# Kernel tuning notes

Measured on AMD Instinct MI355X. Metric: run time of the kernel, lower is better.

Reference implementation:

```python
import jax, jax.numpy as jnp
import numpy as np

S, B, T = 128, 1024, 96
E, H, HH, ATT = 64, 200, 100, 200
ACT, FLD = 32, 8
V_SRC, N_PROD, V_PRIM, N_FLD = 20000, 101, 10000, 64
DEC_IN = ACT + ATT + FLD + H  # 440


def setup_inputs() -> dict:
    key = jax.random.key(0)
    ks = jax.random.split(key, 24)
    rn = lambda k, shp: jax.random.normal(k, shp, dtype=jnp.float32) * 0.05
    sentences = jax.random.randint(ks[0], (S, B), 0, V_SRC)
    is_prod = jax.random.randint(ks[1], (T, B), 0, 2).astype(jnp.int32)
    prod_ids = jax.random.randint(ks[2], (T, B), 0, N_PROD)
    prim_ids = jax.random.randint(ks[3], (T, B), 0, V_PRIM)
    field_ids = jax.random.randint(ks[4], (T, B), 0, N_FLD)
    pt = jax.random.randint(ks[5], (T, B), 0, T)
    parent_t = jnp.minimum(pt, jnp.maximum(jnp.arange(T)[:, None] - 1, 0))  # parent < t
    return {
        'sentences': sentences, 'is_prod': is_prod, 'prod_ids': prod_ids,
        'prim_ids': prim_ids, 'field_ids': field_ids, 'parent_t': parent_t,
        'src_emb': rn(ks[6], (V_SRC, E)),
        'actprod_emb': rn(ks[7], (N_PROD, ACT)),
        'prim_emb': rn(ks[8], (V_PRIM, ACT)),
        'field_emb': rn(ks[9], (N_FLD, FLD)),
        'Wih_f': rn(ks[10], (4 * HH, E)), 'Whh_f': rn(ks[11], (4 * HH, HH)), 'b_f': rn(ks[12], (4 * HH,)),
        'Wih_b': rn(ks[13], (4 * HH, E)), 'Whh_b': rn(ks[14], (4 * HH, HH)), 'b_b': rn(ks[15], (4 * HH,)),
        'Wih_d': rn(ks[16], (4 * H, DEC_IN)), 'Whh_d': rn(ks[17], (4 * H, H)), 'b_d': rn(ks[18], (4 * H,)),
        'W_attn': rn(ks[19], (H, H)),
        'W_av': rn(ks[20], (ATT, 2 * H)),
    }


def _lstm_cell(z, c):
    i, f, g, o = jnp.split(z, 4, axis=-1)  # torch gate order i,f,g,o
    c = jax.nn.sigmoid(f) * c + jax.nn.sigmoid(i) * jnp.tanh(g)
    h = jax.nn.sigmoid(o) * jnp.tanh(c)
    return h, c


def _lstm_dir(x_emb, Wih, Whh, b, reverse):
    # x_emb: [S,B,E]; precompute input projections once
    xw = jnp.einsum('sbe,he->sbh', x_emb, Wih) + b
    nb = x_emb.shape[1]
    hh = Whh.shape[1]
    init = (jnp.zeros((nb, hh), x_emb.dtype), jnp.zeros((nb, hh), x_emb.dtype))
    def step(carry, xw_t):
        h, c = carry
        h, c = _lstm_cell(xw_t + h @ Whh.T, c)
        return (h, c), h
    (hT, cT), hs = jax.lax.scan(step, init, xw, reverse=reverse)
    return hs, hT, cT


def _forward(sentences, is_prod, prod_ids, prim_ids, field_ids, parent_t,
             src_emb, actprod_emb, prim_emb, field_emb,
             Wih_f, Whh_f, b_f, Wih_b, Whh_b, b_b,
             Wih_d, Whh_d, b_d, W_attn, W_av):
    nb = sentences.shape[1]
    nt = is_prod.shape[0]
    emb = src_emb[sentences]                       # [S,B,E]
    hs_f, hTf, cTf = _lstm_dir(emb, Wih_f, Whh_f, b_f, False)
    hs_b, hTb, cTb = _lstm_dir(emb, Wih_b, Whh_b, b_b, True)
    enc = jnp.concatenate([hs_f, hs_b], -1).transpose(1, 0, 2)   # [B,S,H]
    enc_att = enc @ W_attn.T                                     # [B,S,H]
    # replicate torch h0.view(-1, H) on [2,B,HH]
    h = jnp.stack([hTf, hTb]).reshape(-1, H)
    c = jnp.stack([cTf, cTb]).reshape(-1, H)
    Hbuf = jnp.zeros((nt, nb, H), enc.dtype)
    s_att0 = jnp.zeros((nb, ATT), enc.dtype)
    barange = jnp.arange(nb)

    def dec_step(carry, xs):
        h, c, s_att, Hbuf = carry
        t, ip, pid, prid, fid, ptid = xs
        a_tm1 = jnp.where(ip[:, None] == 1, actprod_emb[pid], prim_emb[prid])  # [B,32]
        nft = field_emb[fid]                                                   # [B,8]
        parent = Hbuf[ptid, barange]                                           # [B,H] irregular gather
        inp = jnp.concatenate([a_tm1, s_att, nft, parent], axis=-1)           # [B,440]
        inp = jnp.where(t > 0, inp, jnp.zeros_like(inp))
        h, c = _lstm_cell(inp @ Wih_d.T + h @ Whh_d.T + b_d, c)
        aw = jax.nn.softmax(jnp.einsum('bsh,bh->bs', enc_att, h), axis=-1)
        ctx = jnp.einsum('bs,bsh->bh', aw, enc)
        s_att = jnp.tanh(jnp.concatenate([ctx, h], axis=1) @ W_av.T)
        Hbuf = Hbuf.at[t].set(h)
        return (h, c, s_att, Hbuf), s_att

    xs = (jnp.arange(nt), is_prod, prod_ids, prim_ids, field_ids, parent_t)
    _, att_vecs = jax.lax.scan(dec_step, (h, c, s_att0, Hbuf), xs)
    return att_vecs  # [T,B,ATT]


def reference(sentences, is_prod, prod_ids, prim_ids, field_ids, parent_t,
              src_emb, actprod_emb, prim_emb, field_emb,
              Wih_f, Whh_f, b_f, Wih_b, Whh_b, b_b,
              Wih_d, Whh_d, b_d, W_attn, W_av):
    return _forward(sentences, is_prod, prod_ids, prim_ids, field_ids, parent_t,
                    src_emb, actprod_emb, prim_emb, field_emb,
                    Wih_f, Whh_f, b_f, Wih_b, Whh_b, b_b,
                    Wih_d, Whh_d, b_d, W_attn, W_av)
```

## Files before the change

### kernel.cpp

```cpp
#include <hip/hip_runtime.h>

#define S_LEN 128
#define B_N   1024
#define T_LEN 96
#define E_DIM 64
#define HH    100
#define H_DIM 200
#define ACT_D 32
#define FLD_D 8
#define ATT_D 200
#define DEC_IN 440
#define KTOT  640
#define G4H   800
#define G4HH  400
#define KH_PAD 224
#define KC_PAD 416
#define NCOL_PAD 208
#define EK_ROWS 208
#define XA_LD 648
#define HG_LD 232
#define GA_LD 232
#define CAT_LD 424

typedef unsigned int  u32;
typedef unsigned short u16;
typedef _Float16 f16;
typedef _Float16 f16x8 __attribute__((ext_vector_type(8)));
typedef _Float16 f16x4 __attribute__((ext_vector_type(4)));
typedef float    f32x4 __attribute__((ext_vector_type(4)));

#define MFMA16(a,b,c) __builtin_amdgcn_mfma_f32_16x16x32_f16((a),(b),(c),0,0,0)

static __device__ __forceinline__ float lo_bf(u32 u){ union{u32 i; float f;}v; v.i = u<<16; return v.f; }
static __device__ __forceinline__ float hi_bf(u32 u){ union{u32 i; float f;}v; v.i = u & 0xffff0000u; return v.f; }
static __device__ __forceinline__ float sigf(float x){
  x = fminf(30.f, fmaxf(-30.f, x));
  return 1.f/(1.f + __expf(-x));
}
static __device__ __forceinline__ float tanhf_(float x){
  x = fminf(15.f, fmaxf(-15.f, x));
  float e = __expf(-2.f*x);
  return (1.f - e)/(1.f + e);
}

static __device__ __forceinline__ u16 f2bf(float f){
  union{float f; u32 i;} v; v.f = f;
  u32 r = v.i + 0x7fffu + ((v.i >> 16) & 1u);
  return (u16)(r >> 16);
}
__global__ void k_prep(u16* __restrict__ dst, const float* __restrict__ src,
                       int K, int C, int sk, int sc)
{
  int idx = blockIdx.x*256 + threadIdx.x;
  if (idx >= K*C) return;
  int k = idx / C, c = idx - k*C;
  dst[(size_t)(k>>2)*(4*C) + 4*c + (k&3)] = f2bf(src[(size_t)k*sk + (size_t)c*sc]);
}

__global__ void k_pack16(f16* __restrict__ dst, const float* __restrict__ src,
                         int Kld, int koff, int C, int K, int sk, int sc)
{
  int idx = blockIdx.x*256 + threadIdx.x;
  if (idx >= C*K) return;
  int c = idx / K, k = idx - c*K;
  dst[(size_t)c*Kld + koff + k] = (f16)src[(size_t)k*sk + (size_t)c*sc];
}

__global__ void k_zf16(f16* __restrict__ dst, int n)
{
  int idx = blockIdx.x*256 + threadIdx.x;
  if (idx < n) dst[idx] = (f16)0.f;
}

__global__ __launch_bounds__(256) void k_transpose(
    const f16* __restrict__ enc_sk, f16* __restrict__ enc_ks)
{
  __shared__ f16 ld[H_DIM][136];
  const int b = blockIdx.x, tid = threadIdx.x;
  const f16* src = enc_sk + (size_t)b*S_LEN*H_DIM;
  for (int idx = tid; idx < S_LEN*(H_DIM/4); idx += 256) {
    int s = idx / (H_DIM/4), jc = idx - s*(H_DIM/4);
    f16x4 v = *(const f16x4*)(src + (size_t)s*H_DIM + 4*jc);
    #pragma unroll
    for (int i = 0; i < 4; ++i) ld[4*jc + i][s] = v[i];
  }
  __syncthreads();
  f16* dst = enc_ks + (size_t)b*EK_ROWS*S_LEN;
  for (int idx = tid; idx < H_DIM*(S_LEN/8); idx += 256) {
    int k = idx / (S_LEN/8), so = idx - k*(S_LEN/8);
    f16x8 v;
    #pragma unroll
    for (int i = 0; i < 8; ++i) v[i] = ld[k][8*so + i];
    *(f16x8*)(dst + (size_t)k*S_LEN + 8*so) = v;
  }
}

__global__ __launch_bounds__(512) void k_encoder(
    const int* __restrict__ sentences, const float* __restrict__ src_emb,
    const float* __restrict__ b_f, const float* __restrict__ b_b,
    const uint2* __restrict__ wihF, const uint2* __restrict__ whhF,
    const uint2* __restrict__ wihB, const uint2* __restrict__ whhB,
    f16* __restrict__ enc_sk,
    float* __restrict__ hTf, float* __restrict__ cTf,
    float* __restrict__ hTb, float* __restrict__ cTb)
{
  const int tid = threadIdx.x;
  const int dir = blockIdx.x >> 7;
  const int bg  = blockIdx.x & 127;
  const int b0  = bg * 8;

  __shared__ alignas(16) float xs[8][E_DIM];
  __shared__ alignas(16) float hs[8][HH];
  __shared__ alignas(16) float zs[8][G4HH];

  const uint2* wih = dir ? wihB : wihF;
  const uint2* whh = dir ? whhB : whhF;
  const float* bias = dir ? b_b : b_f;

  for (int idx = tid; idx < 8*HH; idx += 512) ((float*)hs)[idx] = 0.f;
  float c0r = 0.f, c1r = 0.f;

  const int col = tid;
  const bool act = (col < G4HH);
  const float bias0 = act ? bias[col] : 0.f;

  __syncthreads();

  for (int step = 0; step < S_LEN; ++step) {
    const int s = dir ? (S_LEN-1-step) : step;
    {
      int r = tid >> 6, e = tid & 63;
      int tok = sentences[s*B_N + (b0 + r)];
      xs[r][e] = src_emb[(size_t)tok*E_DIM + e];
    }
    __syncthreads();

    if (act) {
      float acc[8];
      #pragma unroll
      for (int r = 0; r < 8; ++r) acc[r] = bias0;
      #pragma unroll 2
      for (int k4 = 0; k4 < E_DIM/4; ++k4) {
        uint2 u = wih[k4*G4HH + col];
        float w0 = lo_bf(u.x), w1 = hi_bf(u.x), w2 = lo_bf(u.y), w3 = hi_bf(u.y);
        #pragma unroll
        for (int r = 0; r < 8; ++r) {
          float4 xv = *(const float4*)&xs[r][4*k4];
          acc[r] += xv.x*w0 + xv.y*w1 + xv.z*w2 + xv.w*w3;
        }
      }
      #pragma unroll 2
      for (int k4 = 0; k4 < HH/4; ++k4) {
        uint2 u = whh[k4*G4HH + col];
        float w0 = lo_bf(u.x), w1 = hi_bf(u.x), w2 = lo_bf(u.y), w3 = hi_bf(u.y);
        #pragma unroll
        for (int r = 0; r < 8; ++r) {
          float4 hv = *(const float4*)&hs[r][4*k4];
          acc[r] += hv.x*w0 + hv.y*w1 + hv.z*w2 + hv.w*w3;
        }
      }
      #pragma unroll
      for (int r = 0; r < 8; ++r) zs[r][col] = acc[r];
    }
    __syncthreads();

    {
      int r = tid / HH, j = tid - r*HH;
      float c = sigf(zs[r][HH+j])*c0r + sigf(zs[r][j])*tanhf_(zs[r][2*HH+j]);
      float h = sigf(zs[r][3*HH+j])*tanhf_(c);
      c0r = c;
      hs[r][j] = h;
      enc_sk[((size_t)(b0+r)*S_LEN + s)*H_DIM + dir*HH + j] = (f16)h;
      if (tid < 8*HH - 512) {
        int idx2 = tid + 512;
        int r2 = idx2 / HH, j2 = idx2 - r2*HH;
        float c2 = sigf(zs[r2][HH+j2])*c1r + sigf(zs[r2][j2])*tanhf_(zs[r2][2*HH+j2]);
        float h2 = sigf(zs[r2][3*HH+j2])*tanhf_(c2);
        c1r = c2;
        hs[r2][j2] = h2;
        enc_sk[((size_t)(b0+r2)*S_LEN + s)*H_DIM + dir*HH + j2] = (f16)h2;
      }
    }
    __syncthreads();
  }

  float* hT = dir ? hTb : hTf;
  float* cT = dir ? cTb : cTf;
  {
    int r = tid / HH, j = tid - r*HH;
    hT[(b0+r)*HH + j] = hs[r][j];
    cT[(b0+r)*HH + j] = c0r;
    if (tid < 8*HH - 512) {
      int idx2 = tid + 512; int r2 = idx2 / HH, j2 = idx2 - r2*HH;
      hT[(b0+r2)*HH + j2] = hs[r2][j2];
      cT[(b0+r2)*HH + j2] = c1r;
    }
  }
}

__global__ __launch_bounds__(512, 2) void k_decoder(
  const int* __restrict__ is_prod, const int* __restrict__ prod_ids,
  const int* __restrict__ prim_ids, const int* __restrict__ field_ids,
  const int* __restrict__ parent_t,
  const float* __restrict__ actprod_emb, const float* __restrict__ prim_emb,
  const float* __restrict__ field_emb, const float* __restrict__ b_d,
  const f16* __restrict__ wall,
  const f16* __restrict__ wattn,
  const f16* __restrict__ wav,
  const f16* __restrict__ enc_ks,
  const float* __restrict__ hTf, const float* __restrict__ cTf,
  const float* __restrict__ hTb, const float* __restrict__ cTb,
  f16* __restrict__ Hbuf, float* __restrict__ out)
{
  const int tid  = threadIdx.x;
  const int lane = tid & 63;
  const int wid  = tid >> 6;
  const int b0   = blockIdx.x * 8;
  const int arow = lane & 15;
  const int aoff = (lane >> 4) * 8;

  __shared__ alignas(16) f16   xa[8][XA_LD];
  __shared__ alignas(16) f16   hg[8][HG_LD];
  __shared__ alignas(16) f16   gA[8][GA_LD];
  __shared__ alignas(16) f16   cat[8][CAT_LD];
  __shared__ alignas(16) f16   aw_sh[8][S_LEN];
  __shared__ alignas(16) float zs[8][G4H];
  __shared__ float biasd[G4H];

  for (int idx = tid; idx < G4H; idx += 512) biasd[idx] = b_d[idx];
  for (int idx = tid; idx < 8*(HG_LD-H_DIM); idx += 512) {
    int n = HG_LD-H_DIM; hg[idx/n][H_DIM + idx%n] = (f16)0.f;
  }
  for (int idx = tid; idx < 8*(GA_LD-H_DIM); idx += 512) {
    int n = GA_LD-H_DIM; gA[idx/n][H_DIM + idx%n] = (f16)0.f;
  }
  for (int idx = tid; idx < 8*(CAT_LD-2*H_DIM); idx += 512) {
    int n = CAT_LD-2*H_DIM; cat[idx/n][2*H_DIM + idx%n] = (f16)0.f;
  }
  for (int idx = tid; idx < 8*ATT_D; idx += 512) {
    xa[idx/ATT_D][ACT_D + idx%ATT_D] = (f16)0.f;
  }
  for (int idx = tid; idx < 8*H_DIM; idx += 512) {
    int r = idx / H_DIM, j = idx - r*H_DIM; int b = b0 + r;
    float v;
    if (b < 512) v = (j < HH) ? hTf[(2*b)*HH + j] : hTf[(2*b+1)*HH + (j-HH)];
    else { int bb = b-512; v = (j < HH) ? hTb[(2*bb)*HH + j] : hTb[(2*bb+1)*HH + (j-HH)]; }
    f16 hv = (f16)v;
    xa[r][DEC_IN + j] = hv; hg[r][j] = hv; cat[r][H_DIM + j] = hv;
  }
  float cst[4];
  #pragma unroll
  for (int kk = 0; kk < 4; ++kk) {
    int slot = tid + 512*kk;
    float v = 0.f;
    if (slot < 8*H_DIM) {
      int r = slot / H_DIM, j = slot - r*H_DIM; int b = b0 + r;
      if (b < 512) v = (j < HH) ? cTf[(2*b)*HH + j] : cTf[(2*b+1)*HH + (j-HH)];
      else { int bb = b-512; v = (j < HH) ? cTb[(2*bb)*HH + j] : cTb[(2*bb+1)*HH + (j-HH)]; }
    }
    cst[kk] = v;
  }
  __syncthreads();

  for (int t = 0; t < T_LEN; ++t) {
    for (int idx = tid; idx < 8*DEC_IN; idx += 512) {
      int r = idx / DEC_IN, k = idx - r*DEC_IN;
      if (k >= ACT_D && k < ACT_D + ATT_D) continue;
      f16 v = (f16)0.f;
      if (t > 0) {
        int b = b0 + r;
        if (k < ACT_D) {
          float f = (is_prod[t*B_N + b] == 1)
            ? actprod_emb[prod_ids[t*B_N + b]*ACT_D + k]
            : prim_emb[prim_ids[t*B_N + b]*ACT_D + k];
          v = (f16)f;
        } else if (k < ACT_D + ATT_D + FLD_D) {
          v = (f16)field_emb[field_ids[t*B_N + b]*FLD_D + (k - ACT_D - ATT_D)];
        } else {
          int pt = parent_t[t*B_N + b];
          v = Hbuf[((size_t)pt*B_N + b)*H_DIM + (k - (ACT_D+ATT_D+FLD_D))];
        }
      }
      xa[r][k] = v;
    }
    __syncthreads();

    {
      f16x8 afr[20];
      #pragma unroll
      for (int kk = 0; kk < 20; ++kk) {
        f16x8 v = {0,0,0,0,0,0,0,0};
        if (arow < 8) v = *(const f16x8*)&xa[arow][kk*32 + aoff];
        afr[kk] = v;
      }
      int t_begin = wid*6 + (wid < 2 ? wid : 2);
      int t_count = 6 + (wid < 2 ? 1 : 0);
      for (int ti = 0; ti < t_count; ti += 2) {
        int ta = t_begin + ti;
        bool hasb = (ti + 1 < t_count);
        int tb = hasb ? ta + 1 : ta;
        int ca = ta*16 + arow;
        int cb = tb*16 + arow;
        float bva = biasd[ca], bvb = biasd[cb];
        f32x4 acca = {bva, bva, bva, bva};
        f32x4 accb = {bvb, bvb, bvb, bvb};
        const f16* pa = wall + (size_t)ca*KTOT + aoff;
        const f16* pb = wall + (size_t)cb*KTOT + aoff;
        #pragma unroll
        for (int kk = 0; kk < 20; ++kk) {
          f16x8 Ba = *(const f16x8*)(pa + kk*32);
          f16x8 Bb = *(const f16x8*)(pb + kk*32);
          acca = MFMA16(afr[kk], Ba, acca);
          accb = MFMA16(afr[kk], Bb, accb);
        }
        if (lane < 32) {
          int rb = (lane >> 4) * 4;
          #pragma unroll
          for (int i2 = 0; i2 < 4; ++i2) zs[rb+i2][ca] = acca[i2];
          if (hasb) {
            #pragma unroll
            for (int i2 = 0; i2 < 4; ++i2) zs[rb+i2][cb] = accb[i2];
          }
        }
      }
    }
    __syncthreads();

    #pragma unroll
    for (int kk = 0; kk < 4; ++kk) {
      int slot = tid + 512*kk;
      if (slot < 8*H_DIM) {
        int r = slot / H_DIM, j = slot - r*H_DIM;
        float c = sigf(zs[r][H_DIM+j])*cst[kk] + sigf(zs[r][j])*tanhf_(zs[r][2*H_DIM+j]);
        float h = sigf(zs[r][3*H_DIM+j])*tanhf_(c);
        cst[kk] = c;
        f16 hv = (f16)h;
        xa[r][DEC_IN + j] = hv; hg[r][j] = hv; cat[r][H_DIM + j] = hv;
        Hbuf[((size_t)t*B_N + (b0+r))*H_DIM + j] = hv;
      }
    }
    __syncthreads();

    {
      f16x8 ga[7];
      #pragma unroll
      for (int kk = 0; kk < 7; ++kk) {
        f16x8 v = {0,0,0,0,0,0,0,0};
        if (arow < 8) v = *(const f16x8*)&hg[arow][kk*32 + aoff];
        ga[kk] = v;
      }
      #pragma unroll
      for (int pass = 0; pass < 2; ++pass) {
        int tt = wid + pass*8;
        if (tt < 13) {
          int c = tt*16 + arow;
          f32x4 acc = {0.f,0.f,0.f,0.f};
          const f16* p = wattn + (size_t)c*KH_PAD + aoff;
          #pragma unroll
          for (int kk = 0; kk < 7; ++kk)
            acc = MFMA16(ga[kk], *(const f16x8*)(p + kk*32), acc);
          if (lane < 32) {
            int rb = (lane >> 4) * 4;
            #pragma unroll
            for (int i2 = 0; i2 < 4; ++i2)
              if (c < H_DIM) gA[rb+i2][c] = (f16)acc[i2];
          }
        }
      }
    }
    __syncthreads();

    {
      const int r = wid;
      const int sl = lane & 15, kp = lane >> 4;
      const f16* ep = enc_ks + ((size_t)(b0+r)*EK_ROWS + kp*52)*S_LEN + 8*sl;
      const f16* gp = &gA[r][kp*52];
      float acc[8] = {0.f,0.f,0.f,0.f,0.f,0.f,0.f,0.f};
      #pragma unroll 4
      for (int i = 0; i < 52; ++i) {
        f16x8 e8 = *(const f16x8*)(ep + (size_t)i*S_LEN);
        float gf = (float)gp[i];
        #pragma unroll
        for (int q = 0; q < 8; ++q) acc[q] += gf * (float)e8[q];
      }
      #pragma unroll
      for (int q = 0; q < 8; ++q) {
        acc[q] += __shfl_xor(acc[q], 16);
        acc[q] += __shfl_xor(acc[q], 32);
      }
      float m = acc[0];
      #pragma unroll
      for (int q = 1; q < 8; ++q) m = fmaxf(m, acc[q]);
      #pragma unroll
      for (int d = 1; d < 16; d <<= 1) m = fmaxf(m, __shfl_xor(m, d));
      float e[8], sm = 0.f;
      #pragma unroll
      for (int q = 0; q < 8; ++q) { e[q] = __expf(acc[q] - m); sm += e[q]; }
      #pragma unroll
      for (int d = 1; d < 16; d <<= 1) sm += __shfl_xor(sm, d);
      float rd = 1.f / sm;
      if (kp == 0) {
        f16x8 w;
        #pragma unroll
        for (int q = 0; q < 8; ++q) w[q] = (f16)(e[q] * rd);
        *(f16x8*)&aw_sh[r][8*sl] = w;
      }
    }
    __syncthreads();

    {
      #pragma unroll
      for (int pass = 0; pass < 2; ++pass) {
        int tt = wid + pass*8;
        if (tt < 13) {
          int c = tt*16 + arow;
          f32x4 acc = {0.f,0.f,0.f,0.f};
          const f16* eb = enc_ks + (size_t)b0*EK_ROWS*S_LEN + (size_t)c*S_LEN + aoff;
          #pragma unroll 4
          for (int kt = 0; kt < 32; ++kt) {
            int rp = kt >> 2;
            int s0 = (kt & 3) * 32;
            f16x8 a = {0,0,0,0,0,0,0,0};
            if (arow == rp) a = *(const f16x8*)&aw_sh[rp][s0 + aoff];
            f16x8 bf = *(const f16x8*)(eb + (size_t)rp*EK_ROWS*S_LEN + s0);
            acc = MFMA16(a, bf, acc);
          }
          if (lane < 32 && c < H_DIM) {
            int rb = (lane >> 4) * 4;
            #pragma unroll
            for (int i2 = 0; i2 < 4; ++i2) cat[rb+i2][c] = (f16)acc[i2];
          }
        }
      }
    }
    __syncthreads();

    {
      f16x8 sa[13];
      #pragma unroll
      for (int kk = 0; kk < 13; ++kk) {
        f16x8 v = {0,0,0,0,0,0,0,0};
        if (arow < 8) v = *(const f16x8*)&cat[arow][kk*32 + aoff];
        sa[kk] = v;
      }
      #pragma unroll
      for (int pass = 0; pass < 2; ++pass) {
        int tt = wid + pass*8;
        if (tt < 13) {
          int c = tt*16 + arow;
          f32x4 acc = {0.f,0.f,0.f,0.f};
          const f16* p = wav + (size_t)c*KC_PAD + aoff;
          #pragma unroll
          for (int kk = 0; kk < 13; ++kk)
            acc = MFMA16(sa[kk], *(const f16x8*)(p + kk*32), acc);
          if (lane < 32 && c < ATT_D) {
            int rb = (lane >> 4) * 4;
            #pragma unroll
            for (int i2 = 0; i2 < 4; ++i2) {
              float v = tanhf_(acc[i2]);
              out[((size_t)t*B_N + (b0+rb+i2))*ATT_D + c] = v;
              xa[rb+i2][ACT_D + c] = (f16)v;
            }
          }
        }
      }
    }
    __syncthreads();
  }
}

extern "C" void kernel_launch(void* const* d_in, const int* in_sizes, int n_in,
                              void* d_out, int out_size, void* d_ws, size_t ws_size,
                              hipStream_t stream)
{
  const int*   sentences = (const int*)  d_in[0];
  const int*   is_prod   = (const int*)  d_in[1];
  const int*   prod_ids  = (const int*)  d_in[2];
  const int*   prim_ids  = (const int*)  d_in[3];
  const int*   field_ids = (const int*)  d_in[4];
  const int*   parent_t  = (const int*)  d_in[5];
  const float* src_emb   = (const float*)d_in[6];
  const float* actprod   = (const float*)d_in[7];
  const float* prim_emb  = (const float*)d_in[8];
  const float* field_emb = (const float*)d_in[9];
  const float* Wih_f = (const float*)d_in[10];
  const float* Whh_f = (const float*)d_in[11];
  const float* b_f   = (const float*)d_in[12];
  const float* Wih_b = (const float*)d_in[13];
  const float* Whh_b = (const float*)d_in[14];
  const float* b_b   = (const float*)d_in[15];
  const float* Wih_d = (const float*)d_in[16];
  const float* Whh_d = (const float*)d_in[17];
  const float* b_d   = (const float*)d_in[18];
  const float* W_attn= (const float*)d_in[19];
  const float* W_av  = (const float*)d_in[20];
  (void)in_sizes; (void)n_in; (void)out_size; (void)ws_size;

  char* ws = (char*)d_ws;
  size_t off = 0;
  auto take = [&](size_t bytes) -> void* {
    void* p = ws + off;
    off = (off + bytes + 255) & ~(size_t)255;
    return p;
  };
  u16* wihF = (u16*)take((size_t)64*400*2);
  u16* whhF = (u16*)take((size_t)100*400*2);
  u16* wihB = (u16*)take((size_t)64*400*2);
  u16* whhB = (u16*)take((size_t)100*400*2);
  f16* wall16  = (f16*)take((size_t)800*640*2);
  f16* wattn16 = (f16*)take((size_t)NCOL_PAD*KH_PAD*2);
  f16* wav16   = (f16*)take((size_t)NCOL_PAD*KC_PAD*2);
  f16* enc_sk  = (f16*)take((size_t)B_N*S_LEN*H_DIM*2);
  f16* enc_ks  = (f16*)take((size_t)B_N*EK_ROWS*S_LEN*2);
  float* hTf = (float*)take((size_t)B_N*HH*4);
  float* cTf = (float*)take((size_t)B_N*HH*4);
  float* hTb = (float*)take((size_t)B_N*HH*4);
  float* cTb = (float*)take((size_t)B_N*HH*4);
  f16* Hbuf16 = (f16*)take((size_t)T_LEN*B_N*H_DIM*2);
  float* outp = (float*)d_out;

  auto prep = [&](u16* dst, const float* src, int K, int C, int sk, int sc){
    int n = K*C;
    k_prep<<<(n+255)/256, 256, 0, stream>>>(dst, src, K, C, sk, sc);
  };
  prep(wihF, Wih_f, 64, 400, 1, 64);
  prep(whhF, Whh_f, 100, 400, 1, 100);
  prep(wihB, Wih_b, 64, 400, 1, 64);
  prep(whhB, Whh_b, 100, 400, 1, 100);

  {
    int n;
    n = NCOL_PAD*KH_PAD; k_zf16<<<(n+255)/256,256,0,stream>>>(wattn16, n);
    n = NCOL_PAD*KC_PAD; k_zf16<<<(n+255)/256,256,0,stream>>>(wav16, n);
    n = 800*440; k_pack16<<<(n+255)/256,256,0,stream>>>(wall16, Wih_d, KTOT, 0,   800, 440, 1, 440);
    n = 800*200; k_pack16<<<(n+255)/256,256,0,stream>>>(wall16, Whh_d, KTOT, 440, 800, 200, 1, 200);
    n = 200*200; k_pack16<<<(n+255)/256,256,0,stream>>>(wattn16, W_attn, KH_PAD, 0, 200, 200, 200, 1);
    n = 200*400; k_pack16<<<(n+255)/256,256,0,stream>>>(wav16, W_av, KC_PAD, 0, 200, 400, 1, 400);
  }

  k_encoder<<<256, 512, 0, stream>>>(sentences, src_emb, b_f, b_b,
      (const uint2*)wihF, (const uint2*)whhF, (const uint2*)wihB, (const uint2*)whhB,
      enc_sk, hTf, cTf, hTb, cTb);

  k_transpose<<<B_N, 256, 0, stream>>>(enc_sk, enc_ks);

  k_decoder<<<128, 512, 0, stream>>>(is_prod, prod_ids, prim_ids, field_ids, parent_t,
      actprod, prim_emb, field_emb, b_d,
      wall16, wattn16, wav16,
      enc_ks, hTf, cTf, hTb, cTb, Hbuf16, outp);
}
```

Baseline: 7.847 ms.

## Precompute encoder-side attention projection and halve decoder batch per block

Adds a k_attgemm kernel that precomputes enc @ W_attn once for all source positions. The decoder then scores attention directly against h, which removes the per-step W_attn GEMM and its barrier. The decoder now handles 4 batch rows per block across 256 blocks instead of 8 across 128, to use more CUs. It also prefetches the next step's input gather into the attention phase, removing one sync per step. The costs are an extra precompute pass and buffer, more wasted MFMA rows (4 of 16 used), and twice the total weight streaming from cache.

```diff
diff --git a/kernel.cpp b/kernel.cpp
--- a/kernel.cpp
+++ b/kernel.cpp
@@ -19,7 +19,6 @@
 #define EK_ROWS 208
 #define XA_LD 648
 #define HG_LD 232
-#define GA_LD 232
 #define CAT_LD 424
 
 typedef unsigned int  u32;
@@ -92,6 +91,44 @@
     #pragma unroll
     for (int i = 0; i < 8; ++i) v[i] = ld[k][8*so + i];
     *(f16x8*)(dst + (size_t)k*S_LEN + 8*so) = v;
+  }
+}
+
+__global__ __launch_bounds__(512) void k_attgemm(
+    const f16* __restrict__ enc_sk, const f16* __restrict__ wattnT,
+    f16* __restrict__ enc_att)
+{
+  __shared__ alignas(16) f16 et[S_LEN][KH_PAD];
+  const int b = blockIdx.x, tid = threadIdx.x;
+  const int lane = tid & 63, wid = tid >> 6;
+  const int arow = lane & 15, aoff = (lane >> 4) * 8;
+  const f16* src = enc_sk + (size_t)b*S_LEN*H_DIM;
+  for (int idx = tid; idx < S_LEN*(H_DIM/8); idx += 512) {
+    int s = idx / (H_DIM/8), jo = idx - s*(H_DIM/8);
+    *(f16x8*)&et[s][8*jo] = *(const f16x8*)(src + (size_t)s*H_DIM + 8*jo);
+  }
+  for (int idx = tid; idx < S_LEN*3; idx += 512) {
+    int s = idx / 3, jo = idx - s*3;
+    *(f16x8*)&et[s][H_DIM + 8*jo] = (f16x8){0,0,0,0,0,0,0,0};
+  }
+  __syncthreads();
+  f16x8 af[7];
+  #pragma unroll
+  for (int kk = 0; kk < 7; ++kk)
+    af[kk] = *(const f16x8*)&et[wid*16 + arow][kk*32 + aoff];
+  f16* dstb = enc_att + (size_t)b*EK_ROWS*S_LEN;
+  for (int tt = 0; tt < 13; ++tt) {
+    int c = tt*16 + arow;
+    f32x4 acc = {0.f,0.f,0.f,0.f};
+    const f16* p = wattnT + (size_t)c*KH_PAD + aoff;
+    #pragma unroll
+    for (int kk = 0; kk < 7; ++kk)
+      acc = MFMA16(af[kk], *(const f16x8*)(p + kk*32), acc);
+    int srow = wid*16 + (lane >> 4)*4;
+    f16x4 v;
+    #pragma unroll
+    for (int i = 0; i < 4; ++i) v[i] = (f16)acc[i];
+    *(f16x4*)(dstb + (size_t)c*S_LEN + srow) = v;
   }
 }
 
@@ -205,9 +242,9 @@
   const float* __restrict__ actprod_emb, const float* __restrict__ prim_emb,
   const float* __restrict__ field_emb, const float* __restrict__ b_d,
   const f16* __restrict__ wall,
-  const f16* __restrict__ wattn,
   const f16* __restrict__ wav,
   const f16* __restrict__ enc_ks,
+  const f16* __restrict__ enc_att,
   const float* __restrict__ hTf, const float* __restrict__ cTf,
   const float* __restrict__ hTb, const float* __restrict__ cTb,
   f16* __restrict__ Hbuf, float* __restrict__ out)
@@ -215,32 +252,28 @@
   const int tid  = threadIdx.x;
   const int lane = tid & 63;
   const int wid  = tid >> 6;
-  const int b0   = blockIdx.x * 8;
+  const int b0   = blockIdx.x * 4;
   const int arow = lane & 15;
   const int aoff = (lane >> 4) * 8;
 
-  __shared__ alignas(16) f16   xa[8][XA_LD];
-  __shared__ alignas(16) f16   hg[8][HG_LD];
-  __shared__ alignas(16) f16   gA[8][GA_LD];
-  __shared__ alignas(16) f16   cat[8][CAT_LD];
-  __shared__ alignas(16) f16   aw_sh[8][S_LEN];
-  __shared__ alignas(16) float zs[8][G4H];
+  __shared__ alignas(16) f16   xa[4][XA_LD];
+  __shared__ alignas(16) f16   hg[4][HG_LD];
+  __shared__ alignas(16) f16   cat[4][CAT_LD];
+  __shared__ alignas(16) f16   aw_sh[4][S_LEN];
+  __shared__ alignas(16) float zs[4][G4H];
   __shared__ float biasd[G4H];
 
   for (int idx = tid; idx < G4H; idx += 512) biasd[idx] = b_d[idx];
-  for (int idx = tid; idx < 8*(HG_LD-H_DIM); idx += 512) {
+  for (int idx = tid; idx < 4*(HG_LD-H_DIM); idx += 512) {
     int n = HG_LD-H_DIM; hg[idx/n][H_DIM + idx%n] = (f16)0.f;
   }
-  for (int idx = tid; idx < 8*(GA_LD-H_DIM); idx += 512) {
-    int n = GA_LD-H_DIM; gA[idx/n][H_DIM + idx%n] = (f16)0.f;
-  }
-  for (int idx = tid; idx < 8*(CAT_LD-2*H_DIM); idx += 512) {
+  for (int idx = tid; idx < 4*(CAT_LD-2*H_DIM); idx += 512) {
     int n = CAT_LD-2*H_DIM; cat[idx/n][2*H_DIM + idx%n] = (f16)0.f;
   }
-  for (int idx = tid; idx < 8*ATT_D; idx += 512) {
-    xa[idx/ATT_D][ACT_D + idx%ATT_D] = (f16)0.f;
-  }
-  for (int idx = tid; idx < 8*H_DIM; idx += 512) {
+  for (int idx = tid; idx < 4*DEC_IN; idx += 512) {
+    xa[idx/DEC_IN][idx%DEC_IN] = (f16)0.f;
+  }
+  for (int idx = tid; idx < 4*H_DIM; idx += 512) {
     int r = idx / H_DIM, j = idx - r*H_DIM; int b = b0 + r;
     float v;
     if (b < 512) v = (j < HH) ? hTf[(2*b)*HH + j] : hTf[(2*b+1)*HH + (j-HH)];
@@ -248,88 +281,49 @@
     f16 hv = (f16)v;
     xa[r][DEC_IN + j] = hv; hg[r][j] = hv; cat[r][H_DIM + j] = hv;
   }
-  float cst[4];
+  float cst[2] = {0.f, 0.f};
   #pragma unroll
-  for (int kk = 0; kk < 4; ++kk) {
+  for (int kk = 0; kk < 2; ++kk) {
     int slot = tid + 512*kk;
-    float v = 0.f;
-    if (slot < 8*H_DIM) {
+    if (slot < 4*H_DIM) {
       int r = slot / H_DIM, j = slot - r*H_DIM; int b = b0 + r;
+      float v;
       if (b < 512) v = (j < HH) ? cTf[(2*b)*HH + j] : cTf[(2*b+1)*HH + (j-HH)];
       else { int bb = b-512; v = (j < HH) ? cTb[(2*bb)*HH + j] : cTb[(2*bb+1)*HH + (j-HH)]; }
-    }
-    cst[kk] = v;
+      cst[kk] = v;
+    }
   }
   __syncthreads();
 
   for (int t = 0; t < T_LEN; ++t) {
-    for (int idx = tid; idx < 8*DEC_IN; idx += 512) {
-      int r = idx / DEC_IN, k = idx - r*DEC_IN;
-      if (k >= ACT_D && k < ACT_D + ATT_D) continue;
-      f16 v = (f16)0.f;
-      if (t > 0) {
-        int b = b0 + r;
-        if (k < ACT_D) {
-          float f = (is_prod[t*B_N + b] == 1)
-            ? actprod_emb[prod_ids[t*B_N + b]*ACT_D + k]
-            : prim_emb[prim_ids[t*B_N + b]*ACT_D + k];
-          v = (f16)f;
-        } else if (k < ACT_D + ATT_D + FLD_D) {
-          v = (f16)field_emb[field_ids[t*B_N + b]*FLD_D + (k - ACT_D - ATT_D)];
-        } else {
-          int pt = parent_t[t*B_N + b];
-          v = Hbuf[((size_t)pt*B_N + b)*H_DIM + (k - (ACT_D+ATT_D+FLD_D))];
-        }
-      }
-      xa[r][k] = v;
-    }
-    __syncthreads();
-
     {
       f16x8 afr[20];
       #pragma unroll
       for (int kk = 0; kk < 20; ++kk) {
         f16x8 v = {0,0,0,0,0,0,0,0};
-        if (arow < 8) v = *(const f16x8*)&xa[arow][kk*32 + aoff];
+        if (arow < 4) v = *(const f16x8*)&xa[arow][kk*32 + aoff];
         afr[kk] = v;
       }
-      int t_begin = wid*6 + (wid < 2 ? wid : 2);
-      int t_count = 6 + (wid < 2 ? 1 : 0);
-      for (int ti = 0; ti < t_count; ti += 2) {
-        int ta = t_begin + ti;
-        bool hasb = (ti + 1 < t_count);
-        int tb = hasb ? ta + 1 : ta;
-        int ca = ta*16 + arow;
-        int cb = tb*16 + arow;
-        float bva = biasd[ca], bvb = biasd[cb];
-        f32x4 acca = {bva, bva, bva, bva};
-        f32x4 accb = {bvb, bvb, bvb, bvb};
-        const f16* pa = wall + (size_t)ca*KTOT + aoff;
-        const f16* pb = wall + (size_t)cb*KTOT + aoff;
+      for (int tt = wid; tt < 50; tt += 8) {
+        int c = tt*16 + arow;
+        float bv = biasd[c];
+        f32x4 acc = {bv, bv, bv, bv};
+        const f16* p = wall + (size_t)c*KTOT + aoff;
         #pragma unroll
-        for (int kk = 0; kk < 20; ++kk) {
-          f16x8 Ba = *(const f16x8*)(pa + kk*32);
-          f16x8 Bb = *(const f16x8*)(pb + kk*32);
-          acca = MFMA16(afr[kk], Ba, acca);
-          accb = MFMA16(afr[kk], Bb, accb);
+        for (int kk = 0; kk < 20; ++kk)
+          acc = MFMA16(afr[kk], *(const f16x8*)(p + kk*32), acc);
+        if (lane < 16) {
+          #pragma unroll
+          for (int i2 = 0; i2 < 4; ++i2) zs[i2][c] = acc[i2];
         }
-        if (lane < 32) {
-          int rb = (lane >> 4) * 4;
-          #pragma unroll
-          for (int i2 = 0; i2 < 4; ++i2) zs[rb+i2][ca] = acca[i2];
-          if (hasb) {
-            #pragma unroll
-            for (int i2 = 0; i2 < 4; ++i2) zs[rb+i2][cb] = accb[i2];
-          }
-        }
       }
     }
     __syncthreads();
 
     #pragma unroll
-    for (int kk = 0; kk < 4; ++kk) {
+    for (int kk = 0; kk < 2; ++kk) {
       int slot = tid + 512*kk;
-      if (slot < 8*H_DIM) {
+      if (slot < 4*H_DIM) {
         int r = slot / H_DIM, j = slot - r*H_DIM;
         float c = sigf(zs[r][H_DIM+j])*cst[kk] + sigf(zs[r][j])*tanhf_(zs[r][2*H_DIM+j]);
         float h = sigf(zs[r][3*H_DIM+j])*tanhf_(c);
@@ -341,47 +335,18 @@
     }
     __syncthreads();
 
-    {
-      f16x8 ga[7];
-      #pragma unroll
-      for (int kk = 0; kk < 7; ++kk) {
-        f16x8 v = {0,0,0,0,0,0,0,0};
-        if (arow < 8) v = *(const f16x8*)&hg[arow][kk*32 + aoff];
-        ga[kk] = v;
-      }
-      #pragma unroll
-      for (int pass = 0; pass < 2; ++pass) {
-        int tt = wid + pass*8;
-        if (tt < 13) {
-          int c = tt*16 + arow;
-          f32x4 acc = {0.f,0.f,0.f,0.f};
-          const f16* p = wattn + (size_t)c*KH_PAD + aoff;
-          #pragma unroll
-          for (int kk = 0; kk < 7; ++kk)
-            acc = MFMA16(ga[kk], *(const f16x8*)(p + kk*32), acc);
-          if (lane < 32) {
-            int rb = (lane >> 4) * 4;
-            #pragma unroll
-            for (int i2 = 0; i2 < 4; ++i2)
-              if (c < H_DIM) gA[rb+i2][c] = (f16)acc[i2];
-          }
-        }
-      }
-    }
-    __syncthreads();
-
-    {
+    if (wid < 4) {
       const int r = wid;
       const int sl = lane & 15, kp = lane >> 4;
-      const f16* ep = enc_ks + ((size_t)(b0+r)*EK_ROWS + kp*52)*S_LEN + 8*sl;
-      const f16* gp = &gA[r][kp*52];
+      const f16* ep = enc_att + ((size_t)(b0+r)*EK_ROWS + kp*52)*S_LEN + 8*sl;
+      const f16* hp = &hg[r][kp*52];
       float acc[8] = {0.f,0.f,0.f,0.f,0.f,0.f,0.f,0.f};
       #pragma unroll 4
       for (int i = 0; i < 52; ++i) {
         f16x8 e8 = *(const f16x8*)(ep + (size_t)i*S_LEN);
-        float gf = (float)gp[i];
+        float hf = (float)hp[i];
         #pragma unroll
-        for (int q = 0; q < 8; ++q) acc[q] += gf * (float)e8[q];
+        for (int q = 0; q < 8; ++q) acc[q] += hf * (float)e8[q];
       }
       #pragma unroll
       for (int q = 0; q < 8; ++q) {
@@ -417,7 +382,7 @@
           f32x4 acc = {0.f,0.f,0.f,0.f};
           const f16* eb = enc_ks + (size_t)b0*EK_ROWS*S_LEN + (size_t)c*S_LEN + aoff;
           #pragma unroll 4
-          for (int kt = 0; kt < 32; ++kt) {
+          for (int kt = 0; kt < 16; ++kt) {
             int rp = kt >> 2;
             int s0 = (kt & 3) * 32;
             f16x8 a = {0,0,0,0,0,0,0,0};
@@ -425,13 +390,33 @@
             f16x8 bf = *(const f16x8*)(eb + (size_t)rp*EK_ROWS*S_LEN + s0);
             acc = MFMA16(a, bf, acc);
           }
-          if (lane < 32 && c < H_DIM) {
-            int rb = (lane >> 4) * 4;
+          if (lane < 16 && c < H_DIM) {
             #pragma unroll
-            for (int i2 = 0; i2 < 4; ++i2) cat[rb+i2][c] = (f16)acc[i2];
+            for (int i2 = 0; i2 < 4; ++i2) cat[i2][c] = (f16)acc[i2];
           }
         }
       }
+      if (t + 1 < T_LEN) {
+        const int tn = t + 1;
+        for (int idx = tid; idx < 4*DEC_IN; idx += 512) {
+          int r = idx / DEC_IN, k = idx - r*DEC_IN;
+          if (k >= ACT_D && k < ACT_D + ATT_D) continue;
+          int b = b0 + r;
+          f16 v;
+          if (k < ACT_D) {
+            float f = (is_prod[tn*B_N + b] == 1)
+              ? actprod_emb[prod_ids[tn*B_N + b]*ACT_D + k]
+              : prim_emb[prim_ids[tn*B_N + b]*ACT_D + k];
+            v = (f16)f;
+          } else if (k < ACT_D + ATT_D + FLD_D) {
+            v = (f16)field_emb[field_ids[tn*B_N + b]*FLD_D + (k - ACT_D - ATT_D)];
+          } else {
+            int pt = parent_t[tn*B_N + b];
+            v = Hbuf[((size_t)pt*B_N + b)*H_DIM + (k - (ACT_D+ATT_D+FLD_D))];
+          }
+          xa[r][k] = v;
+        }
+      }
     }
     __syncthreads();
 
@@ -440,7 +425,7 @@
       #pragma unroll
       for (int kk = 0; kk < 13; ++kk) {
         f16x8 v = {0,0,0,0,0,0,0,0};
-        if (arow < 8) v = *(const f16x8*)&cat[arow][kk*32 + aoff];
+        if (arow < 4) v = *(const f16x8*)&cat[arow][kk*32 + aoff];
         sa[kk] = v;
       }
       #pragma unroll
@@ -453,13 +438,12 @@
           #pragma unroll
           for (int kk = 0; kk < 13; ++kk)
             acc = MFMA16(sa[kk], *(const f16x8*)(p + kk*32), acc);
-          if (lane < 32 && c < ATT_D) {
-            int rb = (lane >> 4) * 4;
+          if (lane < 16 && c < ATT_D) {
             #pragma unroll
             for (int i2 = 0; i2 < 4; ++i2) {
               float v = tanhf_(acc[i2]);
-              out[((size_t)t*B_N + (b0+rb+i2))*ATT_D + c] = v;
-              xa[rb+i2][ACT_D + c] = (f16)v;
+              out[((size_t)t*B_N + (b0+i2))*ATT_D + c] = v;
+              xa[i2][ACT_D + c] = (f16)v;
             }
           }
         }
@@ -508,10 +492,11 @@
   u16* wihB = (u16*)take((size_t)64*400*2);
   u16* whhB = (u16*)take((size_t)100*400*2);
   f16* wall16  = (f16*)take((size_t)800*640*2);
-  f16* wattn16 = (f16*)take((size_t)NCOL_PAD*KH_PAD*2);
+  f16* wattnT  = (f16*)take((size_t)NCOL_PAD*KH_PAD*2);
   f16* wav16   = (f16*)take((size_t)NCOL_PAD*KC_PAD*2);
   f16* enc_sk  = (f16*)take((size_t)B_N*S_LEN*H_DIM*2);
   f16* enc_ks  = (f16*)take((size_t)B_N*EK_ROWS*S_LEN*2);
+  f16* enc_att = (f16*)take((size_t)B_N*EK_ROWS*S_LEN*2);
   float* hTf = (float*)take((size_t)B_N*HH*4);
   float* cTf = (float*)take((size_t)B_N*HH*4);
   float* hTb = (float*)take((size_t)B_N*HH*4);
@@ -530,11 +515,11 @@
 
   {
     int n;
-    n = NCOL_PAD*KH_PAD; k_zf16<<<(n+255)/256,256,0,stream>>>(wattn16, n);
+    n = NCOL_PAD*KH_PAD; k_zf16<<<(n+255)/256,256,0,stream>>>(wattnT, n);
     n = NCOL_PAD*KC_PAD; k_zf16<<<(n+255)/256,256,0,stream>>>(wav16, n);
     n = 800*440; k_pack16<<<(n+255)/256,256,0,stream>>>(wall16, Wih_d, KTOT, 0,   800, 440, 1, 440);
     n = 800*200; k_pack16<<<(n+255)/256,256,0,stream>>>(wall16, Whh_d, KTOT, 440, 800, 200, 1, 200);
-    n = 200*200; k_pack16<<<(n+255)/256,256,0,stream>>>(wattn16, W_attn, KH_PAD, 0, 200, 200, 200, 1);
+    n = 200*200; k_pack16<<<(n+255)/256,256,0,stream>>>(wattnT, W_attn, KH_PAD, 0, 200, 200, 1, 200);
     n = 200*400; k_pack16<<<(n+255)/256,256,0,stream>>>(wav16, W_av, KC_PAD, 0, 200, 400, 1, 400);
   }
 
@@ -543,9 +528,10 @@
       enc_sk, hTf, cTf, hTb, cTb);
 
   k_transpose<<<B_N, 256, 0, stream>>>(enc_sk, enc_ks);
-
-  k_decoder<<<128, 512, 0, stream>>>(is_prod, prod_ids, prim_ids, field_ids, parent_t,
+  k_attgemm<<<B_N, 512, 0, stream>>>(enc_sk, wattnT, enc_att);
+
+  k_decoder<<<256, 512, 0, stream>>>(is_prod, prod_ids, prim_ids, field_ids, parent_t,
       actprod, prim_emb, field_emb, b_d,
-      wall16, wattn16, wav16,
-      enc_ks, hTf, cTf, hTb, cTb, Hbuf16, outp);
-}
+      wall16, wav16,
+      enc_ks, enc_att, hTf, cTf, hTb, cTb, Hbuf16, outp);
+}
```

Result: faster. 6.673 ms (-15.0%).
